# Performance work log

Hardware: AMD Instinct MI355X
Metric: run time of the kernel (lower is better)

Reference implementation:

```python
import jax, jax.numpy as jnp
import numpy as np

N = 50000      # num_labels (nodes)
HID = 64       # hidden_dim
HEADS = 4
CH = 16        # hidden_dim // 4 per head
R = 4          # relations
E = 200000     # edges per relation
DEPTH = 2
SLOPE = 0.2    # GATv2 leaky_relu negative slope
EPS = 1e-5     # LayerNorm eps


def layer_norm(x, g, b):
    mu = jnp.mean(x, axis=-1, keepdims=True)
    var = jnp.mean((x - mu) ** 2, axis=-1, keepdims=True)
    return (x - mu) / jnp.sqrt(var + EPS) * g + b


def setup_inputs() -> dict:
    key = jax.random.key(0)
    ks = jax.random.split(key, 8)
    # edges with src != dst (PyG remove_self_loops is then a no-op)
    src = jax.random.randint(ks[0], (R, E), 0, N, dtype=jnp.int32)
    off = jax.random.randint(ks[1], (R, E), 1, N, dtype=jnp.int32)
    dst = ((src + off) % N).astype(jnp.int32)
    edge_index = jnp.stack([src, dst], axis=1)  # [R, 2, E]
    s = 1.0 / np.sqrt(HID)
    return {
        "label_embeddings": jax.random.normal(ks[2], (N, HID), jnp.float32) * 0.5,
        "entry_w": jax.random.normal(ks[3], (HID, HID), jnp.float32) * s,
        "entry_b": jnp.zeros((HID,), jnp.float32),
        "entry_ln_g": jnp.ones((HID,), jnp.float32),
        "entry_ln_b": jnp.zeros((HID,), jnp.float32),
        "conv_wl": jax.random.normal(ks[4], (DEPTH, R, HID, HEADS * CH), jnp.float32) * s,
        "conv_wr": jax.random.normal(ks[5], (DEPTH, R, HID, HEADS * CH), jnp.float32) * s,
        "conv_att": jax.random.normal(ks[6], (DEPTH, R, HEADS, CH), jnp.float32) * (1.0 / np.sqrt(CH)),
        "conv_bias": jnp.zeros((DEPTH, R, HEADS * CH), jnp.float32),
        "norm_g": jnp.ones((HID,), jnp.float32),
        "norm_b": jnp.zeros((HID,), jnp.float32),
        "edge_index": edge_index,
    }


def _gatv2_layer(x, wl, wr, att, bias, src, dst):
    """One GATv2Conv over one relation. x:[N,HID]; returns [N, HEADS*CH]."""
    xl = (x @ wl).reshape(N, HEADS, CH)  # source transform
    xr = (x @ wr).reshape(N, HEADS, CH)  # target transform
    m = xl[src] + xr[dst]                          # [E+N, HEADS, CH]
    e = jnp.einsum('ehc,hc->eh', jax.nn.leaky_relu(m, SLOPE), att)  # [E+N, HEADS]
    # segment softmax over incoming edges of each dst node
    emax = jax.ops.segment_max(e, dst, num_segments=N)  # [N, HEADS]
    a = jnp.exp(e - emax[dst])
    denom = jax.ops.segment_sum(a, dst, num_segments=N)
    alpha = a / denom[dst]                          # every node has a self-loop -> denom > 0
    msg = xl[src] * alpha[..., None]                # [E+N, HEADS, CH]
    out = jax.ops.segment_sum(msg, dst, num_segments=N).reshape(N, HEADS * CH)
    return out + bias


def reference(label_embeddings, entry_w, entry_b, entry_ln_g, entry_ln_b,
              conv_wl, conv_wr, conv_att, conv_bias, norm_g, norm_b, edge_index):
    x = jax.nn.gelu(layer_norm(label_embeddings @ entry_w + entry_b, entry_ln_g, entry_ln_b),
                    approximate=False)
    loop = jnp.arange(N, dtype=edge_index.dtype)
    for layer in range(DEPTH):
        outs = []
        for r in range(R):
            src = jnp.concatenate([edge_index[r, 0], loop])  # add self-loops (PyG default)
            dst = jnp.concatenate([edge_index[r, 1], loop])
            outs.append(_gatv2_layer(x, conv_wl[layer, r], conv_wr[layer, r],
                                     conv_att[layer, r], conv_bias[layer, r], src, dst))
        x = sum(outs) / R                              # HeteroConv aggr='mean'
        x = layer_norm(jax.nn.gelu(x, approximate=False), norm_g, norm_b)  # dropout = identity (eval)
    return x
```

## Files before the change

kernel.cpp:

```cpp
#include <hip/hip_runtime.h>
#include <hip/hip_bf16.h>

#define NN 50000
#define RR 4
#define EE 200000
#define CAP 32

typedef __hip_bfloat16 bf16;
typedef __attribute__((ext_vector_type(8))) short short8;
typedef __attribute__((ext_vector_type(4))) float float4v;
typedef __attribute__((ext_vector_type(2))) float float2v;

__device__ __forceinline__ float b2f(bf16 v) { return __bfloat162float(v); }
__device__ __forceinline__ unsigned short f2bu(float v) {
    bf16 h = __float2bfloat16(v);
    return *(unsigned short*)&h;
}
__device__ __forceinline__ float ldf(const void* p, int i, int isbf) {
    return isbf ? __bfloat162float(((const bf16*)p)[i]) : ((const float*)p)[i];
}
__device__ __forceinline__ int dtype_isbf(const void* lg) {
    return ((const unsigned*)lg)[0] == 0x3F803F80u;
}
__device__ __forceinline__ float gelu_exact(float x) {
    return 0.5f * x * (1.0f + erff(x * 0.70710678118654752f));
}
__device__ __forceinline__ float lrelu(float m) { return fmaxf(m, 0.2f * m); }
__device__ __forceinline__ float2v bp2(unsigned u) {
    float2v f;
    f.x = __uint_as_float(u << 16);
    f.y = __uint_as_float(u & 0xffff0000u);
    return f;
}
__device__ __forceinline__ float2v lrelu2(float2v m) {
    float2v s = m * 0.2f;
    float2v r;
    r.x = fmaxf(m.x, s.x);
    r.y = fmaxf(m.y, s.y);
    return r;
}

#define PW_ENTRY_W 0
#define PW_ENTRY_B 4096
#define PW_LN_G    4160
#define PW_LN_B    4224
#define PW_WL      4288
#define PW_ATT     69824
#define PW_BIAS    70336
#define PW_NG      70848
#define PW_NB      70912
#define PW_TOT     70976

#define WT_ELEMS (2 * RR * 128 * 64)

__global__ __launch_bounds__(256) void cvt_k(const void* ew, const void* eb, const void* lg,
                                             const void* lb, const void* wl, const void* wr,
                                             const void* at, const void* bi, const void* ng,
                                             const void* nb,
                                             float* __restrict__ P, bf16* __restrict__ WT,
                                             int* __restrict__ cnt) {
    int i = blockIdx.x * 256 + threadIdx.x;
    int isbf = dtype_isbf(lg);
    if (i < RR * NN) cnt[i] = 0;
    if (i < WT_ELEMS) {
        int k = i & 63;
        int c = (i >> 6) & 127;
        int lr = i >> 13;
        float v = (c < 64) ? ldf(wl, (lr * 64 + k) * 64 + c, isbf)
                           : ldf(wr, (lr * 64 + k) * 64 + (c - 64), isbf);
        WT[i] = __float2bfloat16(v);
    }
    if (i < PW_TOT) {
        const void* src = nullptr;
        int off = 0;
        if (i < PW_ENTRY_B)      { src = ew; off = i - PW_ENTRY_W; }
        else if (i < PW_LN_G)    { src = eb; off = i - PW_ENTRY_B; }
        else if (i < PW_LN_B)    { src = lg; off = i - PW_LN_G; }
        else if (i < PW_WL)      { src = lb; off = i - PW_LN_B; }
        else if (i < PW_ATT)     { src = nullptr; }
        else if (i < PW_BIAS)    { src = at; off = i - PW_ATT; }
        else if (i < PW_NG)      { src = bi; off = i - PW_BIAS; }
        else if (i < PW_NB)      { src = ng; off = i - PW_NG; }
        else                     { src = nb; off = i - PW_NB; }
        if (src) P[i] = ldf(src, off, isbf);
    }
}

__global__ void scatter_k(const int* __restrict__ ei, int* __restrict__ cnt,
                          int* __restrict__ col) {
    int e = blockIdx.x * 256 + threadIdx.x;
    int r = blockIdx.y;
    if (e < EE) {
        int s = ei[r * 2 * EE + e];
        int d = ei[r * 2 * EE + EE + e];
        int p = atomicAdd(&cnt[r * NN + d], 1);
        if (p < CAP) col[((size_t)r * NN + d) * CAP + p] = s;
    }
}

__global__ __launch_bounds__(256) void entry_k(const void* __restrict__ emb,
                                               const void* __restrict__ lg,
                                               const float* __restrict__ P,
                                               bf16* __restrict__ xout) {
    int wave = (blockIdx.x * 256 + threadIdx.x) >> 6;
    int c = threadIdx.x & 63;
    if (wave >= NN) return;
    int isbf = dtype_isbf(lg);
    float ev = ldf(emb, wave * 64 + c, isbf);
    float acc = 0.f;
#pragma unroll 8
    for (int k = 0; k < 64; k++) {
        float xv = __shfl(ev, k, 64);
        acc += xv * P[PW_ENTRY_W + k * 64 + c];
    }
    acc += P[PW_ENTRY_B + c];
    float s = acc;
#pragma unroll
    for (int m = 1; m < 64; m <<= 1) s += __shfl_xor(s, m, 64);
    float mu = s * (1.f / 64.f);
    float d = acc - mu;
    float vs = d * d;
#pragma unroll
    for (int m = 1; m < 64; m <<= 1) vs += __shfl_xor(vs, m, 64);
    float var = vs * (1.f / 64.f);
    float y = d * rsqrtf(var + 1e-5f) * P[PW_LN_G + c] + P[PW_LN_B + c];
    xout[wave * 64 + c] = __float2bfloat16(gelu_exact(y));
}

#define GR 80
__global__ __launch_bounds__(256) void gemm_m(const bf16* __restrict__ X,
                                              const bf16* __restrict__ WTlayer,
                                              bf16* __restrict__ xlB,
                                              bf16* __restrict__ xrB) {
    int r = blockIdx.y;
    const short* Xs = (const short*)X;
    const short* WT = (const short*)(WTlayer + (size_t)r * 8192);
    bf16* xl = xlB + (size_t)r * NN * 64;
    bf16* xr = xrB + (size_t)r * NN * 64;

    __shared__ float sh[16 * 132];
    int t = threadIdx.x;
    int w = t >> 6;
    int lane = t & 63;
    int m = lane & 15, kq = lane >> 4;
    int row0 = blockIdx.x * GR;

    short8 b0[2], b1[2];
    int c0t[2];
#pragma unroll
    for (int tile = 0; tile < 2; tile++) {
        int ct = w * 2 + tile;
        int c0 = ct * 16 + m;
        c0t[tile] = c0;
        const short* bp = WT + c0 * 64 + kq * 8;
        b0[tile] = *(const short8*)bp;
        b1[tile] = *(const short8*)(bp + 32);
    }

    const short* ap = Xs + (row0 + m) * 64 + kq * 8;
    short8 a0 = *(const short8*)ap;
    short8 a1 = *(const short8*)(ap + 32);

    for (int g = 0; g < 5; g++) {
        short8 na0, na1;
        if (g < 4) {
            const short* np = ap + (g + 1) * 16 * 64;
            na0 = *(const short8*)np;
            na1 = *(const short8*)(np + 32);
        }
#pragma unroll
        for (int tile = 0; tile < 2; tile++) {
            float4v acc = {0.f, 0.f, 0.f, 0.f};
            asm volatile(
                "v_mfma_f32_16x16x32_bf16 %0, %1, %2, %0\n\t"
                "v_mfma_f32_16x16x32_bf16 %0, %3, %4, %0\n\t"
                "s_nop 7\n\t"
                "s_nop 7"
                : "+v"(acc)
                : "v"(a0), "v"(b0[tile]), "v"(a1), "v"(b1[tile]));
#pragma unroll
            for (int i = 0; i < 4; i++) sh[(kq * 4 + i) * 132 + c0t[tile]] = acc[i];
        }
        __syncthreads();
        {
            int row = t >> 4, cg = (t & 15) * 8;
            float v0 = sh[row * 132 + cg + 0], v1 = sh[row * 132 + cg + 1];
            float v2 = sh[row * 132 + cg + 2], v3 = sh[row * 132 + cg + 3];
            float v4 = sh[row * 132 + cg + 4], v5 = sh[row * 132 + cg + 5];
            float v6 = sh[row * 132 + cg + 6], v7 = sh[row * 132 + cg + 7];
            uint4 u;
            u.x = ((unsigned)f2bu(v1) << 16) | f2bu(v0);
            u.y = ((unsigned)f2bu(v3) << 16) | f2bu(v2);
            u.z = ((unsigned)f2bu(v5) << 16) | f2bu(v4);
            u.w = ((unsigned)f2bu(v7) << 16) | f2bu(v6);
            size_t grow = row0 + g * 16 + row;
            if (cg < 64) *(uint4*)&xl[grow * 64 + cg] = u;
            else         *(uint4*)&xr[grow * 64 + (cg - 64)] = u;
        }
        __syncthreads();
        a0 = na0; a1 = na1;
    }
}

__device__ __forceinline__ void edge_accum(uint4 u0, uint4 u1, bool act,
                                           const float2v at2[8], const float2v xr2[8],
                                           float2v A2[8], float& D) {
    float2v x2[8];
    x2[0] = bp2(u0.x); x2[1] = bp2(u0.y); x2[2] = bp2(u0.z); x2[3] = bp2(u0.w);
    x2[4] = bp2(u1.x); x2[5] = bp2(u1.y); x2[6] = bp2(u1.z); x2[7] = bp2(u1.w);
    float2v t2 = (float2v){0.f, 0.f};
#pragma unroll
    for (int i = 0; i < 8; i++)
        t2 = t2 + lrelu2(x2[i] + xr2[i]) * at2[i];
    float tt = t2.x + t2.y;
    float p = act ? exp2f(tt) : 0.f;
    D += p;
    float2v p2 = (float2v){p, p};
#pragma unroll
    for (int i = 0; i < 8; i++) A2[i] = A2[i] + p2 * x2[i];
}

__global__ __launch_bounds__(256) void aggfin_k(const bf16* __restrict__ xlB,
                                                const bf16* __restrict__ xrB,
                                                const float* __restrict__ attL,
                                                const float* __restrict__ biasL,
                                                const int* __restrict__ cnt,
                                                const int* __restrict__ col,
                                                const float* __restrict__ P,
                                                const void* __restrict__ lg,
                                                void* __restrict__ outp,
                                                int finalOut) {
    __shared__ float shRes[RR][4][68];
    int t = threadIdx.x;
    int r = t >> 6;
    int lane = t & 63;
    int nodeBase = blockIdx.x * 4;
    int nn = lane >> 4, es = (lane >> 2) & 3, h = lane & 3;
    int node = nodeBase + nn;

    const unsigned* xl = (const unsigned*)(xlB + (size_t)r * NN * 64);
    const unsigned* xr = (const unsigned*)(xrB + (size_t)r * NN * 64);
    const float* att = attL + r * 64;
    const float* bias = biasL + r * 64;
    const int* bucket = col + ((size_t)r * NN + node) * CAP;

    int cn_raw = cnt[r * NN + node];
    int c0raw = (es > 0) ? bucket[es - 1] : node;
    int c1raw = bucket[es + 3];
    const uint4* qr = (const uint4*)(xr + (size_t)node * 32 + h * 8);
    uint4 r0 = qr[0], r1 = qr[1];

    unsigned s0 = (unsigned)c0raw < (unsigned)NN ? (unsigned)c0raw : (unsigned)(NN - 1);
    unsigned s1 = (unsigned)c1raw < (unsigned)NN ? (unsigned)c1raw : (unsigned)(NN - 1);
    const uint4* q0 = (const uint4*)(xl + (size_t)s0 * 32 + h * 8);
    uint4 u0 = q0[0], u1 = q0[1];
    const uint4* q1 = (const uint4*)(xl + (size_t)s1 * 32 + h * 8);
    uint4 w0 = q1[0], w1 = q1[1];

    float2v at2[8], xr2[8];
    {
        const float4* apv = (const float4*)(att + h * 16);
#pragma unroll
        for (int i = 0; i < 4; i++) {
            float4 a = apv[i];
            at2[2 * i].x = a.x * 1.44269504f; at2[2 * i].y = a.y * 1.44269504f;
            at2[2 * i + 1].x = a.z * 1.44269504f; at2[2 * i + 1].y = a.w * 1.44269504f;
        }
        xr2[0] = bp2(r0.x); xr2[1] = bp2(r0.y); xr2[2] = bp2(r0.z); xr2[3] = bp2(r0.w);
        xr2[4] = bp2(r1.x); xr2[5] = bp2(r1.y); xr2[6] = bp2(r1.z); xr2[7] = bp2(r1.w);
    }
    int cn = cn_raw > CAP ? CAP : cn_raw;
    int total = cn + 1;
    int kmax = total;
    kmax = max(kmax, __shfl_xor(kmax, 16, 64));
    kmax = max(kmax, __shfl_xor(kmax, 32, 64));

    float2v A2[8];
#pragma unroll
    for (int i = 0; i < 8; i++) A2[i] = (float2v){0.f, 0.f};
    float D = 0.f;

    edge_accum(u0, u1, es < total, at2, xr2, A2, D);
    edge_accum(w0, w1, es + 4 < total, at2, xr2, A2, D);

    for (int k = es + 8; k < kmax; k += 4) {
        bool act = k < total;
        int sr = act ? bucket[k - 1] : node;
        const uint4* q = (const uint4*)(xl + (size_t)sr * 32 + h * 8);
        uint4 t0 = q[0], t1 = q[1];
        edge_accum(t0, t1, act, at2, xr2, A2, D);
    }

    D += __shfl_xor(D, 4, 64);
    D += __shfl_xor(D, 8, 64);
#pragma unroll
    for (int i = 0; i < 8; i++) {
        A2[i].x += __shfl_xor(A2[i].x, 4, 64);
        A2[i].x += __shfl_xor(A2[i].x, 8, 64);
        A2[i].y += __shfl_xor(A2[i].y, 4, 64);
        A2[i].y += __shfl_xor(A2[i].y, 8, 64);
    }
    if (es == 0) {
        float inv = __builtin_amdgcn_rcpf(D);
        const float4* bp = (const float4*)(bias + h * 16);
        float* dst = &shRes[r][nn][h * 16];
#pragma unroll
        for (int i = 0; i < 4; i++) {
            float4 b = bp[i];
            dst[4 * i + 0] = A2[2 * i].x * inv + b.x;
            dst[4 * i + 1] = A2[2 * i].y * inv + b.y;
            dst[4 * i + 2] = A2[2 * i + 1].x * inv + b.z;
            dst[4 * i + 3] = A2[2 * i + 1].y * inv + b.w;
        }
    }
    __syncthreads();
    int wn = t >> 6, c = t & 63;
    float v = shRes[0][wn][c] + shRes[1][wn][c] + shRes[2][wn][c] + shRes[3][wn][c];
    v = gelu_exact(v * 0.25f);
    float s = v;
#pragma unroll
    for (int m = 1; m < 64; m <<= 1) s += __shfl_xor(s, m, 64);
    float mu = s * (1.f / 64.f);
    float d = v - mu;
    float vs = d * d;
#pragma unroll
    for (int m = 1; m < 64; m <<= 1) vs += __shfl_xor(vs, m, 64);
    float var = vs * (1.f / 64.f);
    float y = d * rsqrtf(var + 1e-5f) * P[PW_NG + c] + P[PW_NB + c];
    size_t o = (size_t)(nodeBase + wn) * 64 + c;
    if (!finalOut) {
        ((bf16*)outp)[o] = __float2bfloat16(y);
    } else {
        if (dtype_isbf(lg)) ((bf16*)outp)[o] = __float2bfloat16(y);
        else                ((float*)outp)[o] = y;
    }
}

extern "C" void kernel_launch(void* const* d_in, const int* in_sizes, int n_in,
                              void* d_out, int out_size, void* d_ws, size_t ws_size,
                              hipStream_t stream) {
    const void* emb = d_in[0];
    const void* lg  = d_in[3];
    const int*  ei  = (const int*)d_in[11];

    const size_t BUF = (size_t)NN * 64;

    bf16* X   = (bf16*)d_ws;
    bf16* XL  = X + BUF;
    bf16* XR  = XL + RR * BUF;
    bf16* WT  = XR + RR * BUF;
    float* P  = (float*)(WT + WT_ELEMS);
    int* cnt  = (int*)(P + PW_TOT);
    int* col  = cnt + RR * NN;

    int cvtN = RR * NN;
    cvt_k<<<(cvtN + 255) / 256, 256, 0, stream>>>(d_in[1], d_in[2], d_in[3], d_in[4],
                                                  d_in[5], d_in[6], d_in[7], d_in[8],
                                                  d_in[9], d_in[10], P, WT, cnt);
    scatter_k<<<dim3((EE + 255) / 256, RR), 256, 0, stream>>>(ei, cnt, col);

    int nodeBlocks = (NN + 3) / 4;
    int gemmBlocks = NN / GR;

    entry_k<<<nodeBlocks, 256, 0, stream>>>(emb, lg, P, X);

    for (int l = 0; l < 2; l++) {
        gemm_m<<<dim3(gemmBlocks, RR), 256, 0, stream>>>(X, WT + (size_t)l * RR * 8192, XL, XR);
        aggfin_k<<<nodeBlocks, 256, 0, stream>>>(
            XL, XR, P + PW_ATT + (size_t)l * RR * 64, P + PW_BIAS + (size_t)l * RR * 64,
            cnt, col, P, lg, (l == 0) ? (void*)X : d_out, l);
    }
}
```

Baseline: 324.0 us.

## Make aggregation and entry kernels persistent with software-pipelined gathers

The aggregation kernel changes from one block per 4 nodes to a fixed grid of 1250 blocks, each handling 10 node groups. The next group's count, bucket, xr and first neighbour loads are issued while the current group computes, so gather latency is hidden by software prefetching rather than by occupancy. The entry kernel is likewise made persistent with a one-node-ahead prefetch of the embedding row. The cost is higher register pressure, possibly lower occupancy, and less latency hiding across waves, since each block serialises groups separated by barriers.

```diff
diff --git a/kernel.cpp b/kernel.cpp
--- a/kernel.cpp
+++ b/kernel.cpp
@@ -25,7 +25,6 @@
 __device__ __forceinline__ float gelu_exact(float x) {
     return 0.5f * x * (1.0f + erff(x * 0.70710678118654752f));
 }
-__device__ __forceinline__ float lrelu(float m) { return fmaxf(m, 0.2f * m); }
 __device__ __forceinline__ float2v bp2(unsigned u) {
     float2v f;
     f.x = __uint_as_float(u << 16);
@@ -98,33 +97,40 @@
     }
 }
 
+#define EGRID 625
+#define EWAVES (EGRID * 4)
+#define ENODES (NN / EWAVES)
 __global__ __launch_bounds__(256) void entry_k(const void* __restrict__ emb,
                                                const void* __restrict__ lg,
                                                const float* __restrict__ P,
                                                bf16* __restrict__ xout) {
-    int wave = (blockIdx.x * 256 + threadIdx.x) >> 6;
+    int wid = (blockIdx.x * 256 + threadIdx.x) >> 6;
     int c = threadIdx.x & 63;
-    if (wave >= NN) return;
     int isbf = dtype_isbf(lg);
-    float ev = ldf(emb, wave * 64 + c, isbf);
-    float acc = 0.f;
+    float ev_next = ldf(emb, wid * 64 + c, isbf);
+    for (int j = 0; j < ENODES; ++j) {
+        int node = wid + j * EWAVES;
+        float ev = ev_next;
+        if (j < ENODES - 1) ev_next = ldf(emb, (node + EWAVES) * 64 + c, isbf);
+        float acc = 0.f;
 #pragma unroll 8
-    for (int k = 0; k < 64; k++) {
-        float xv = __shfl(ev, k, 64);
-        acc += xv * P[PW_ENTRY_W + k * 64 + c];
-    }
-    acc += P[PW_ENTRY_B + c];
-    float s = acc;
-#pragma unroll
-    for (int m = 1; m < 64; m <<= 1) s += __shfl_xor(s, m, 64);
-    float mu = s * (1.f / 64.f);
-    float d = acc - mu;
-    float vs = d * d;
-#pragma unroll
-    for (int m = 1; m < 64; m <<= 1) vs += __shfl_xor(vs, m, 64);
-    float var = vs * (1.f / 64.f);
-    float y = d * rsqrtf(var + 1e-5f) * P[PW_LN_G + c] + P[PW_LN_B + c];
-    xout[wave * 64 + c] = __float2bfloat16(gelu_exact(y));
+        for (int k = 0; k < 64; k++) {
+            float xv = __shfl(ev, k, 64);
+            acc += xv * P[PW_ENTRY_W + k * 64 + c];
+        }
+        acc += P[PW_ENTRY_B + c];
+        float s = acc;
+#pragma unroll
+        for (int m = 1; m < 64; m <<= 1) s += __shfl_xor(s, m, 64);
+        float mu = s * (1.f / 64.f);
+        float d = acc - mu;
+        float vs = d * d;
+#pragma unroll
+        for (int m = 1; m < 64; m <<= 1) vs += __shfl_xor(vs, m, 64);
+        float var = vs * (1.f / 64.f);
+        float y = d * rsqrtf(var + 1e-5f) * P[PW_LN_G + c] + P[PW_LN_B + c];
+        xout[node * 64 + c] = __float2bfloat16(gelu_exact(y));
+    }
 }
 
 #define GR 80
@@ -202,6 +208,47 @@
     }
 }
 
+#define AGRID 1250
+#define AGROUPS 10
+
+struct Front { int cn; int c0; int c1; uint4 xa, xb; };
+struct Gath  { uint4 u0, u1, w0, w1; int total; };
+
+__device__ __forceinline__ Front issueA(const int* __restrict__ cntr,
+                                        const int* __restrict__ colr,
+                                        const unsigned* __restrict__ xr,
+                                        int node, int es, int h) {
+    Front f;
+    f.cn = cntr[node];
+    const int* bucket = colr + (size_t)node * CAP;
+    f.c0 = (es > 0) ? bucket[es - 1] : node;
+    f.c1 = bucket[es + 3];
+    const uint4* qr = (const uint4*)(xr + (size_t)node * 32 + h * 8);
+    f.xa = qr[0];
+    f.xb = qr[1];
+    return f;
+}
+
+__device__ __forceinline__ Gath issueB(const Front& f, const unsigned* __restrict__ xl,
+                                       int node, int es, int h) {
+    Gath g;
+    int cn = f.cn > CAP ? CAP : f.cn;
+    g.total = cn + 1;
+    bool act0 = es < g.total;
+    bool act1 = es + 4 < g.total;
+    unsigned s0 = act0 ? (unsigned)f.c0 : (unsigned)node;
+    unsigned s1 = act1 ? (unsigned)f.c1 : (unsigned)node;
+    if (s0 >= NN) s0 = NN - 1;
+    if (s1 >= NN) s1 = NN - 1;
+    const uint4* q0 = (const uint4*)(xl + (size_t)s0 * 32 + h * 8);
+    g.u0 = q0[0];
+    g.u1 = q0[1];
+    const uint4* q1 = (const uint4*)(xl + (size_t)s1 * 32 + h * 8);
+    g.w0 = q1[0];
+    g.w1 = q1[1];
+    return g;
+}
+
 __device__ __forceinline__ void edge_accum(uint4 u0, uint4 u1, bool act,
                                            const float2v at2[8], const float2v xr2[8],
                                            float2v A2[8], float& D) {
@@ -234,30 +281,19 @@
     int t = threadIdx.x;
     int r = t >> 6;
     int lane = t & 63;
-    int nodeBase = blockIdx.x * 4;
     int nn = lane >> 4, es = (lane >> 2) & 3, h = lane & 3;
-    int node = nodeBase + nn;
+    int gBase = blockIdx.x;
 
     const unsigned* xl = (const unsigned*)(xlB + (size_t)r * NN * 64);
     const unsigned* xr = (const unsigned*)(xrB + (size_t)r * NN * 64);
+    const int* cntr = cnt + r * NN;
+    const int* colr = col + (size_t)r * NN * CAP;
     const float* att = attL + r * 64;
     const float* bias = biasL + r * 64;
-    const int* bucket = col + ((size_t)r * NN + node) * CAP;
-
-    int cn_raw = cnt[r * NN + node];
-    int c0raw = (es > 0) ? bucket[es - 1] : node;
-    int c1raw = bucket[es + 3];
-    const uint4* qr = (const uint4*)(xr + (size_t)node * 32 + h * 8);
-    uint4 r0 = qr[0], r1 = qr[1];
-
-    unsigned s0 = (unsigned)c0raw < (unsigned)NN ? (unsigned)c0raw : (unsigned)(NN - 1);
-    unsigned s1 = (unsigned)c1raw < (unsigned)NN ? (unsigned)c1raw : (unsigned)(NN - 1);
-    const uint4* q0 = (const uint4*)(xl + (size_t)s0 * 32 + h * 8);
-    uint4 u0 = q0[0], u1 = q0[1];
-    const uint4* q1 = (const uint4*)(xl + (size_t)s1 * 32 + h * 8);
-    uint4 w0 = q1[0], w1 = q1[1];
-
-    float2v at2[8], xr2[8];
+
+#define NODE_OF(gi) ((gBase + (gi) * AGRID) * 4 + nn)
+
+    float2v at2[8];
     {
         const float4* apv = (const float4*)(att + h * 16);
 #pragma unroll
@@ -266,74 +302,112 @@
             at2[2 * i].x = a.x * 1.44269504f; at2[2 * i].y = a.y * 1.44269504f;
             at2[2 * i + 1].x = a.z * 1.44269504f; at2[2 * i + 1].y = a.w * 1.44269504f;
         }
-        xr2[0] = bp2(r0.x); xr2[1] = bp2(r0.y); xr2[2] = bp2(r0.z); xr2[3] = bp2(r0.w);
-        xr2[4] = bp2(r1.x); xr2[5] = bp2(r1.y); xr2[6] = bp2(r1.z); xr2[7] = bp2(r1.w);
-    }
-    int cn = cn_raw > CAP ? CAP : cn_raw;
-    int total = cn + 1;
-    int kmax = total;
-    kmax = max(kmax, __shfl_xor(kmax, 16, 64));
-    kmax = max(kmax, __shfl_xor(kmax, 32, 64));
-
-    float2v A2[8];
-#pragma unroll
-    for (int i = 0; i < 8; i++) A2[i] = (float2v){0.f, 0.f};
-    float D = 0.f;
-
-    edge_accum(u0, u1, es < total, at2, xr2, A2, D);
-    edge_accum(w0, w1, es + 4 < total, at2, xr2, A2, D);
-
-    for (int k = es + 8; k < kmax; k += 4) {
-        bool act = k < total;
-        int sr = act ? bucket[k - 1] : node;
-        const uint4* q = (const uint4*)(xl + (size_t)sr * 32 + h * 8);
-        uint4 t0 = q[0], t1 = q[1];
-        edge_accum(t0, t1, act, at2, xr2, A2, D);
-    }
-
-    D += __shfl_xor(D, 4, 64);
-    D += __shfl_xor(D, 8, 64);
-#pragma unroll
-    for (int i = 0; i < 8; i++) {
-        A2[i].x += __shfl_xor(A2[i].x, 4, 64);
-        A2[i].x += __shfl_xor(A2[i].x, 8, 64);
-        A2[i].y += __shfl_xor(A2[i].y, 4, 64);
-        A2[i].y += __shfl_xor(A2[i].y, 8, 64);
-    }
-    if (es == 0) {
-        float inv = __builtin_amdgcn_rcpf(D);
-        const float4* bp = (const float4*)(bias + h * 16);
-        float* dst = &shRes[r][nn][h * 16];
-#pragma unroll
-        for (int i = 0; i < 4; i++) {
-            float4 b = bp[i];
-            dst[4 * i + 0] = A2[2 * i].x * inv + b.x;
-            dst[4 * i + 1] = A2[2 * i].y * inv + b.y;
-            dst[4 * i + 2] = A2[2 * i + 1].x * inv + b.z;
-            dst[4 * i + 3] = A2[2 * i + 1].y * inv + b.w;
-        }
-    }
-    __syncthreads();
-    int wn = t >> 6, c = t & 63;
-    float v = shRes[0][wn][c] + shRes[1][wn][c] + shRes[2][wn][c] + shRes[3][wn][c];
-    v = gelu_exact(v * 0.25f);
-    float s = v;
-#pragma unroll
-    for (int m = 1; m < 64; m <<= 1) s += __shfl_xor(s, m, 64);
-    float mu = s * (1.f / 64.f);
-    float d = v - mu;
-    float vs = d * d;
-#pragma unroll
-    for (int m = 1; m < 64; m <<= 1) vs += __shfl_xor(vs, m, 64);
-    float var = vs * (1.f / 64.f);
-    float y = d * rsqrtf(var + 1e-5f) * P[PW_NG + c] + P[PW_NB + c];
-    size_t o = (size_t)(nodeBase + wn) * 64 + c;
-    if (!finalOut) {
-        ((bf16*)outp)[o] = __float2bfloat16(y);
-    } else {
-        if (dtype_isbf(lg)) ((bf16*)outp)[o] = __float2bfloat16(y);
-        else                ((float*)outp)[o] = y;
-    }
+    }
+    int isbf = finalOut ? dtype_isbf(lg) : 1;
+
+    Front fA = issueA(cntr, colr, xr, NODE_OF(0), es, h);
+    Gath  gA = issueB(fA, xl, NODE_OF(0), es, h);
+    Front fB = issueA(cntr, colr, xr, NODE_OF(1), es, h);
+
+    for (int it = 0; it < AGROUPS / 2; ++it) {
+        int giE = 2 * it, giO = 2 * it + 1;
+        bool more = it < AGROUPS / 2 - 1;
+
+        Front fC, fD;
+        if (more) fC = issueA(cntr, colr, xr, NODE_OF(giE + 2), es, h);
+        Gath gB = issueB(fB, xl, NODE_OF(giO), es, h);
+
+#pragma unroll 1
+        for (int half = 0; half < 2; ++half) {
+            const Gath&  G = half ? gB : gA;
+            const Front& F = half ? fB : fA;
+            int gi = half ? giO : giE;
+            int node = half ? NODE_OF(giO) : NODE_OF(giE);
+
+            if (half) {
+                if (more) {
+                    fD = issueA(cntr, colr, xr, NODE_OF(giO + 2), es, h);
+                    gA = issueB(fC, xl, NODE_OF(giE + 2), es, h);
+                }
+            }
+
+            float2v xr2[8];
+            xr2[0] = bp2(F.xa.x); xr2[1] = bp2(F.xa.y); xr2[2] = bp2(F.xa.z); xr2[3] = bp2(F.xa.w);
+            xr2[4] = bp2(F.xb.x); xr2[5] = bp2(F.xb.y); xr2[6] = bp2(F.xb.z); xr2[7] = bp2(F.xb.w);
+
+            int total = G.total;
+            int kmax = total;
+            kmax = max(kmax, __shfl_xor(kmax, 16, 64));
+            kmax = max(kmax, __shfl_xor(kmax, 32, 64));
+
+            float2v A2[8];
+#pragma unroll
+            for (int i = 0; i < 8; i++) A2[i] = (float2v){0.f, 0.f};
+            float D = 0.f;
+
+            edge_accum(G.u0, G.u1, es < total, at2, xr2, A2, D);
+            edge_accum(G.w0, G.w1, es + 4 < total, at2, xr2, A2, D);
+
+            const int* bucket = colr + (size_t)node * CAP;
+            for (int k = es + 8; k < kmax; k += 4) {
+                bool act = k < total;
+                int sr = act ? bucket[k - 1] : node;
+                const uint4* q = (const uint4*)(xl + (size_t)sr * 32 + h * 8);
+                uint4 t0 = q[0], t1 = q[1];
+                edge_accum(t0, t1, act, at2, xr2, A2, D);
+            }
+
+            D += __shfl_xor(D, 4, 64);
+            D += __shfl_xor(D, 8, 64);
+#pragma unroll
+            for (int i = 0; i < 8; i++) {
+                A2[i].x += __shfl_xor(A2[i].x, 4, 64);
+                A2[i].x += __shfl_xor(A2[i].x, 8, 64);
+                A2[i].y += __shfl_xor(A2[i].y, 4, 64);
+                A2[i].y += __shfl_xor(A2[i].y, 8, 64);
+            }
+            if (es == 0) {
+                float inv = __builtin_amdgcn_rcpf(D);
+                const float4* bp = (const float4*)(bias + h * 16);
+                float* dst = &shRes[r][nn][h * 16];
+#pragma unroll
+                for (int i = 0; i < 4; i++) {
+                    float4 b = bp[i];
+                    dst[4 * i + 0] = A2[2 * i].x * inv + b.x;
+                    dst[4 * i + 1] = A2[2 * i].y * inv + b.y;
+                    dst[4 * i + 2] = A2[2 * i + 1].x * inv + b.z;
+                    dst[4 * i + 3] = A2[2 * i + 1].y * inv + b.w;
+                }
+            }
+            __syncthreads();
+            {
+                int wn = t >> 6, c = t & 63;
+                float v = shRes[0][wn][c] + shRes[1][wn][c] + shRes[2][wn][c] + shRes[3][wn][c];
+                v = gelu_exact(v * 0.25f);
+                float s = v;
+#pragma unroll
+                for (int m = 1; m < 64; m <<= 1) s += __shfl_xor(s, m, 64);
+                float mu = s * (1.f / 64.f);
+                float d = v - mu;
+                float vs = d * d;
+#pragma unroll
+                for (int m = 1; m < 64; m <<= 1) vs += __shfl_xor(vs, m, 64);
+                float var = vs * (1.f / 64.f);
+                float y = d * rsqrtf(var + 1e-5f) * P[PW_NG + c] + P[PW_NB + c];
+                int nodeBase = (gBase + gi * AGRID) * 4;
+                size_t o = (size_t)(nodeBase + wn) * 64 + c;
+                if (!finalOut) {
+                    ((bf16*)outp)[o] = __float2bfloat16(y);
+                } else {
+                    if (isbf) ((bf16*)outp)[o] = __float2bfloat16(y);
+                    else      ((float*)outp)[o] = y;
+                }
+            }
+            __syncthreads();
+        }
+        if (more) { fA = fC; fB = fD; }
+    }
+#undef NODE_OF
 }
 
 extern "C" void kernel_launch(void* const* d_in, const int* in_sizes, int n_in,
@@ -359,14 +433,13 @@
                                                   d_in[9], d_in[10], P, WT, cnt);
     scatter_k<<<dim3((EE + 255) / 256, RR), 256, 0, stream>>>(ei, cnt, col);
 
-    int nodeBlocks = (NN + 3) / 4;
     int gemmBlocks = NN / GR;
 
-    entry_k<<<nodeBlocks, 256, 0, stream>>>(emb, lg, P, X);
+    entry_k<<<EGRID, 256, 0, stream>>>(emb, lg, P, X);
 
     for (int l = 0; l < 2; l++) {
         gemm_m<<<dim3(gemmBlocks, RR), 256, 0, stream>>>(X, WT + (size_t)l * RR * 8192, XL, XR);
-        aggfin_k<<<nodeBlocks, 256, 0, stream>>>(
+        aggfin_k<<<AGRID, 256, 0, stream>>>(
             XL, XR, P + PW_ATT + (size_t)l * RR * 64, P + PW_BIAS + (size_t)l * RR * 64,
             cnt, col, P, lg, (l == 0) ? (void*)X : d_out, l);
     }
```

Result: slower. 388.4 us (+19.9%).

## Fuse edge scatter with entry MLP and store neighbor indices as 16-bit

Applied to the files above, without the earlier changes.

Merges the CSR bucket scatter and the entry linear+LayerNorm+GELU into one kernel launch, using separate block ranges for each task. Bucket column indices are stored as unsigned short, which halves index traffic in the aggregation kernel. The conversion kernel now uses 1024-thread blocks. The 16-bit indices rely on the node count being below 65536, and the fused kernel fixes grid sizes to the compile-time constants.

```diff
diff --git a/kernel.cpp b/kernel.cpp
--- a/kernel.cpp
+++ b/kernel.cpp
@@ -25,7 +25,6 @@
 __device__ __forceinline__ float gelu_exact(float x) {
     return 0.5f * x * (1.0f + erff(x * 0.70710678118654752f));
 }
-__device__ __forceinline__ float lrelu(float m) { return fmaxf(m, 0.2f * m); }
 __device__ __forceinline__ float2v bp2(unsigned u) {
     float2v f;
     f.x = __uint_as_float(u << 16);
@@ -53,13 +52,13 @@
 
 #define WT_ELEMS (2 * RR * 128 * 64)
 
-__global__ __launch_bounds__(256) void cvt_k(const void* ew, const void* eb, const void* lg,
-                                             const void* lb, const void* wl, const void* wr,
-                                             const void* at, const void* bi, const void* ng,
-                                             const void* nb,
-                                             float* __restrict__ P, bf16* __restrict__ WT,
-                                             int* __restrict__ cnt) {
-    int i = blockIdx.x * 256 + threadIdx.x;
+__global__ __launch_bounds__(1024) void cvt_k(const void* ew, const void* eb, const void* lg,
+                                              const void* lb, const void* wl, const void* wr,
+                                              const void* at, const void* bi, const void* ng,
+                                              const void* nb,
+                                              float* __restrict__ P, bf16* __restrict__ WT,
+                                              int* __restrict__ cnt) {
+    int i = blockIdx.x * 1024 + threadIdx.x;
     int isbf = dtype_isbf(lg);
     if (i < RR * NN) cnt[i] = 0;
     if (i < WT_ELEMS) {
@@ -86,45 +85,58 @@
     }
 }
 
-__global__ void scatter_k(const int* __restrict__ ei, int* __restrict__ cnt,
-                          int* __restrict__ col) {
-    int e = blockIdx.x * 256 + threadIdx.x;
-    int r = blockIdx.y;
-    if (e < EE) {
-        int s = ei[r * 2 * EE + e];
-        int d = ei[r * 2 * EE + EE + e];
-        int p = atomicAdd(&cnt[r * NN + d], 1);
-        if (p < CAP) col[((size_t)r * NN + d) * CAP + p] = s;
-    }
-}
-
-__global__ __launch_bounds__(256) void entry_k(const void* __restrict__ emb,
+#define SCAT_BLOCKS 782
+#define ENTRY_BLOCKS 2500
+#define ENTRY_WAVES (ENTRY_BLOCKS * 4)
+__global__ __launch_bounds__(256) void scent_k(const int* __restrict__ ei,
+                                               int* __restrict__ cnt,
+                                               unsigned short* __restrict__ col,
+                                               const void* __restrict__ emb,
                                                const void* __restrict__ lg,
                                                const float* __restrict__ P,
                                                bf16* __restrict__ xout) {
-    int wave = (blockIdx.x * 256 + threadIdx.x) >> 6;
+    int b = blockIdx.x;
+    if (b < SCAT_BLOCKS) {
+        int base = b * 1024 + threadIdx.x;
+#pragma unroll
+        for (int j = 0; j < 4; j++) {
+            int idx = base + j * 256;
+            if (idx < RR * EE) {
+                int r = idx / EE;
+                int e = idx - r * EE;
+                int s = ei[r * 2 * EE + e];
+                int d = ei[r * 2 * EE + EE + e];
+                int p = atomicAdd(&cnt[r * NN + d], 1);
+                if (p < CAP) col[((size_t)r * NN + d) * CAP + p] = (unsigned short)s;
+            }
+        }
+        return;
+    }
+    int wv = (b - SCAT_BLOCKS) * 4 + (threadIdx.x >> 6);
     int c = threadIdx.x & 63;
-    if (wave >= NN) return;
     int isbf = dtype_isbf(lg);
-    float ev = ldf(emb, wave * 64 + c, isbf);
-    float acc = 0.f;
+    for (int j = 0; j < 5; j++) {
+        int node = wv + j * ENTRY_WAVES;
+        float ev = ldf(emb, node * 64 + c, isbf);
+        float acc = 0.f;
 #pragma unroll 8
-    for (int k = 0; k < 64; k++) {
-        float xv = __shfl(ev, k, 64);
-        acc += xv * P[PW_ENTRY_W + k * 64 + c];
-    }
-    acc += P[PW_ENTRY_B + c];
-    float s = acc;
-#pragma unroll
-    for (int m = 1; m < 64; m <<= 1) s += __shfl_xor(s, m, 64);
-    float mu = s * (1.f / 64.f);
-    float d = acc - mu;
-    float vs = d * d;
-#pragma unroll
-    for (int m = 1; m < 64; m <<= 1) vs += __shfl_xor(vs, m, 64);
-    float var = vs * (1.f / 64.f);
-    float y = d * rsqrtf(var + 1e-5f) * P[PW_LN_G + c] + P[PW_LN_B + c];
-    xout[wave * 64 + c] = __float2bfloat16(gelu_exact(y));
+        for (int k = 0; k < 64; k++) {
+            float xv = __shfl(ev, k, 64);
+            acc += xv * P[PW_ENTRY_W + k * 64 + c];
+        }
+        acc += P[PW_ENTRY_B + c];
+        float s = acc;
+#pragma unroll
+        for (int m = 1; m < 64; m <<= 1) s += __shfl_xor(s, m, 64);
+        float mu = s * (1.f / 64.f);
+        float d = acc - mu;
+        float vs = d * d;
+#pragma unroll
+        for (int m = 1; m < 64; m <<= 1) vs += __shfl_xor(vs, m, 64);
+        float var = vs * (1.f / 64.f);
+        float y = d * rsqrtf(var + 1e-5f) * P[PW_LN_G + c] + P[PW_LN_B + c];
+        xout[node * 64 + c] = __float2bfloat16(gelu_exact(y));
+    }
 }
 
 #define GR 80
@@ -225,7 +237,7 @@
                                                 const float* __restrict__ attL,
                                                 const float* __restrict__ biasL,
                                                 const int* __restrict__ cnt,
-                                                const int* __restrict__ col,
+                                                const unsigned short* __restrict__ col,
                                                 const float* __restrict__ P,
                                                 const void* __restrict__ lg,
                                                 void* __restrict__ outp,
@@ -242,11 +254,11 @@
     const unsigned* xr = (const unsigned*)(xrB + (size_t)r * NN * 64);
     const float* att = attL + r * 64;
     const float* bias = biasL + r * 64;
-    const int* bucket = col + ((size_t)r * NN + node) * CAP;
+    const unsigned short* bucket = col + ((size_t)r * NN + node) * CAP;
 
     int cn_raw = cnt[r * NN + node];
-    int c0raw = (es > 0) ? bucket[es - 1] : node;
-    int c1raw = bucket[es + 3];
+    int c0raw = (es > 0) ? (int)bucket[es - 1] : node;
+    int c1raw = (int)bucket[es + 3];
     const uint4* qr = (const uint4*)(xr + (size_t)node * 32 + h * 8);
     uint4 r0 = qr[0], r1 = qr[1];
 
@@ -285,7 +297,7 @@
 
     for (int k = es + 8; k < kmax; k += 4) {
         bool act = k < total;
-        int sr = act ? bucket[k - 1] : node;
+        int sr = act ? (int)bucket[k - 1] : node;
         const uint4* q = (const uint4*)(xl + (size_t)sr * 32 + h * 8);
         uint4 t0 = q[0], t1 = q[1];
         edge_accum(t0, t1, act, at2, xr2, A2, D);
@@ -351,18 +363,17 @@
     bf16* WT  = XR + RR * BUF;
     float* P  = (float*)(WT + WT_ELEMS);
     int* cnt  = (int*)(P + PW_TOT);
-    int* col  = cnt + RR * NN;
+    unsigned short* col = (unsigned short*)(cnt + RR * NN);
 
     int cvtN = RR * NN;
-    cvt_k<<<(cvtN + 255) / 256, 256, 0, stream>>>(d_in[1], d_in[2], d_in[3], d_in[4],
-                                                  d_in[5], d_in[6], d_in[7], d_in[8],
-                                                  d_in[9], d_in[10], P, WT, cnt);
-    scatter_k<<<dim3((EE + 255) / 256, RR), 256, 0, stream>>>(ei, cnt, col);
-
-    int nodeBlocks = (NN + 3) / 4;
+    cvt_k<<<(cvtN + 1023) / 1024, 1024, 0, stream>>>(d_in[1], d_in[2], d_in[3], d_in[4],
+                                                     d_in[5], d_in[6], d_in[7], d_in[8],
+                                                     d_in[9], d_in[10], P, WT, cnt);
+
+    scent_k<<<SCAT_BLOCKS + ENTRY_BLOCKS, 256, 0, stream>>>(ei, cnt, col, emb, lg, P, X);
+
     int gemmBlocks = NN / GR;
-
-    entry_k<<<nodeBlocks, 256, 0, stream>>>(emb, lg, P, X);
+    int nodeBlocks = NN / 4;
 
     for (int l = 0; l < 2; l++) {
         gemm_m<<<dim3(gemmBlocks, RR), 256, 0, stream>>>(X, WT + (size_t)l * RR * 8192, XL, XR);
```

Measured after the change: 334.8 us. 1.03x slower.
